# Kernel tuning notes

Measured on AMD Instinct MI355X. Metric: run time of the kernel, lower is better.

## Reference

```python
import jax, jax.numpy as jnp
import numpy as np

SIZE = 1024        # number of neurons
INPUT = 1024       # input_size (previous layer width)
CTX = 512          # context_size
CMS = 4            # context_map_size -> 2**4 = 16 weight rows per neuron
BATCH = 256
LR = 0.01
PCLIP = 0.01       # pred_clipping
WCLIP = 5.0        # weight_clipping


def _logit(x):
    return jnp.log(x) - jnp.log1p(-x)


def setup_inputs() -> dict:
    key = jax.random.key(0)
    k1, k2, k3, k4, k5, k6 = jax.random.split(key, 6)
    logits = jax.random.normal(k1, (INPUT, BATCH), jnp.float32)
    context_inputs = jax.random.normal(k2, (CTX, BATCH), jnp.float32)
    targets = jax.random.uniform(k3, (BATCH,), jnp.float32)
    context_maps = jax.random.normal(k4, (SIZE, CMS, CTX), jnp.float32)
    context_maps = context_maps / jnp.linalg.norm(context_maps, axis=2, keepdims=True)
    context_bias = jax.random.normal(k5, (SIZE, CMS, 1), jnp.float32)
    lo = _logit(jnp.float32(PCLIP))
    hi = _logit(jnp.float32(1.0 - PCLIP))
    bias = jax.random.uniform(k6, (1,), jnp.float32, lo, hi)
    weights = jnp.full((SIZE, 2 ** CMS, INPUT), 1.0 / INPUT, jnp.float32)
    return dict(logits=logits, context_inputs=context_inputs, targets=targets,
                weights=weights, context_maps=context_maps,
                context_bias=context_bias, bias=bias)


def reference(logits, context_inputs, targets, weights, context_maps, context_bias, bias):
    # --- context hashing: which of the 2^CMS weight rows each (neuron, sample) uses ---
    # distances: (size, cms, batch)
    distances = jnp.einsum('smc,cb->smb', context_maps, context_inputs)
    bits = (distances > context_bias).astype(jnp.int32)
    conv = (2 ** jnp.arange(CMS, dtype=jnp.int32))[None, :, None]
    idx = jnp.sum(bits * conv, axis=1)                 # (size, batch) in [0, 2^CMS)

    rows = jnp.arange(SIZE)[:, None]                   # (size, 1)
    sel = weights[rows, idx]                           # gathered weights (size, batch, input)

    lo = _logit(jnp.float32(PCLIP))
    hi = _logit(jnp.float32(1.0 - PCLIP))
    # torch does matmul(sel, logits).diagonal(dim1=1,dim2=2); the diagonal is exactly
    # the per-sample dot product, computed here directly without the (size,b,b) waste.
    out = jnp.clip(jnp.einsum('sbi,ib->sb', sel, logits), lo, hi)
    out = out.at[0].set(bias[0])                       # bias overrides neuron 0

    # --- online weight update (targets provided) ---
    sig = jax.nn.sigmoid(out)                          # (size, batch)
    upd = LR * (sig - targets[None, :])[:, :, None] * logits.T[None, :, :]  # (size,b,input)
    new_weights = weights.at[rows, idx].set(jnp.clip(sel - upd, -WCLIP, WCLIP))

    return jnp.squeeze(out), new_weights
```

## Files before the change

### kernel.cpp

```cpp
#include <hip/hip_runtime.h>

#define LRC   0.01f
#define WCLIP 5.0f
#define LO   (-4.5951198501345898f)
#define HI   ( 4.5951198501345898f)

__device__ __forceinline__ unsigned short f2bf(float f) {
    unsigned int u = __float_as_uint(f);
    u += 0x7fffu + ((u >> 16) & 1u);
    return (unsigned short)(u >> 16);
}
__device__ __forceinline__ float bflo(unsigned int p) { return __uint_as_float(p << 16); }
__device__ __forceinline__ float bfhi(unsigned int p) { return __uint_as_float(p & 0xffff0000u); }

__global__ __launch_bounds__(256) void k1_idx_lt(
    const float* __restrict__ cmap,
    const float* __restrict__ ctx,
    const float* __restrict__ cbias,
    const float* __restrict__ logits,
    int*   __restrict__ idxb,
    float* __restrict__ lT)
{
    __shared__ __align__(16) float As[64 * 68];
    __shared__ __align__(16) float Bs[64 * 68];
    const int t   = threadIdx.x;
    const int blk = blockIdx.x;

    if (blk < 256) {
        const int gm = blk >> 2, gn = blk & 3;
        const int m0 = gm << 6, n0 = gn << 6;
        const int tm = t >> 4, tn = t & 15;

        const int rs = t >> 4;
        const int cs = (t & 15) << 2;

        float acc[4][4];
        #pragma unroll
        for (int i = 0; i < 4; i++)
            #pragma unroll
            for (int j = 0; j < 4; j++) acc[i][j] = 0.f;

        float4 va[4], vb[4];
        #pragma unroll
        for (int rep = 0; rep < 4; rep++) {
            va[rep] = *(const float4*)(cmap + (m0 + (rep << 4) + rs) * 512 + cs);
            vb[rep] = *(const float4*)(ctx + (((rep << 4) + rs)) * 256 + n0 + cs);
        }

        for (int k0 = 0; k0 < 512; k0 += 64) {
            __syncthreads();
            #pragma unroll
            for (int rep = 0; rep < 4; rep++) {
                const int r = (rep << 4) + rs;
                As[(cs + 0) * 68 + r] = va[rep].x;
                As[(cs + 1) * 68 + r] = va[rep].y;
                As[(cs + 2) * 68 + r] = va[rep].z;
                As[(cs + 3) * 68 + r] = va[rep].w;
                *(float4*)(Bs + r * 68 + cs) = vb[rep];
            }
            if (k0 + 64 < 512) {
                #pragma unroll
                for (int rep = 0; rep < 4; rep++) {
                    va[rep] = *(const float4*)(cmap + (m0 + (rep << 4) + rs) * 512 + k0 + 64 + cs);
                    vb[rep] = *(const float4*)(ctx + (k0 + 64 + (rep << 4) + rs) * 256 + n0 + cs);
                }
            }
            __syncthreads();

            const float* ap = As + (tm << 2);
            const float* bp = Bs + (tn << 2);
            #pragma unroll 8
            for (int k = 0; k < 64; ++k) {
                float4 a4 = *(const float4*)(ap + k * 68);
                float4 b4 = *(const float4*)(bp + k * 68);
                acc[0][0] = fmaf(a4.x, b4.x, acc[0][0]);
                acc[0][1] = fmaf(a4.x, b4.y, acc[0][1]);
                acc[0][2] = fmaf(a4.x, b4.z, acc[0][2]);
                acc[0][3] = fmaf(a4.x, b4.w, acc[0][3]);
                acc[1][0] = fmaf(a4.y, b4.x, acc[1][0]);
                acc[1][1] = fmaf(a4.y, b4.y, acc[1][1]);
                acc[1][2] = fmaf(a4.y, b4.z, acc[1][2]);
                acc[1][3] = fmaf(a4.y, b4.w, acc[1][3]);
                acc[2][0] = fmaf(a4.z, b4.x, acc[2][0]);
                acc[2][1] = fmaf(a4.z, b4.y, acc[2][1]);
                acc[2][2] = fmaf(a4.z, b4.z, acc[2][2]);
                acc[2][3] = fmaf(a4.z, b4.w, acc[2][3]);
                acc[3][0] = fmaf(a4.w, b4.x, acc[3][0]);
                acc[3][1] = fmaf(a4.w, b4.y, acc[3][1]);
                acc[3][2] = fmaf(a4.w, b4.z, acc[3][2]);
                acc[3][3] = fmaf(a4.w, b4.w, acc[3][3]);
            }
        }
        const int s = (gm << 4) + tm;
        int4 iv;
        int* ivp = &iv.x;
        float cb[4];
        #pragma unroll
        for (int i = 0; i < 4; i++) cb[i] = cbias[(s << 2) + i];
        #pragma unroll
        for (int j = 0; j < 4; j++) {
            int v = 0;
            #pragma unroll
            for (int i = 0; i < 4; i++)
                v |= (acc[i][j] > cb[i]) ? (1 << i) : 0;
            ivp[j] = v;
        }
        *(int4*)(idxb + s * 256 + n0 + (tn << 2)) = iv;
    } else {
        float* T = As;
        const int bi = blk - 256;
        const int i0 = (bi >> 2) << 6;
        const int b0 = (bi & 3) << 6;
        #pragma unroll
        for (int rep = 0; rep < 4; rep++) {
            int flat4 = rep * 256 + t;
            int r = flat4 >> 4;
            int c = (flat4 & 15) << 2;
            float4 v = *(const float4*)(logits + (i0 + r) * 256 + b0 + c);
            T[(c + 0) * 68 + r] = v.x;
            T[(c + 1) * 68 + r] = v.y;
            T[(c + 2) * 68 + r] = v.z;
            T[(c + 3) * 68 + r] = v.w;
        }
        __syncthreads();
        #pragma unroll
        for (int rep = 0; rep < 4; rep++) {
            int flat4 = rep * 256 + t;
            int r = flat4 >> 4;
            int c = (flat4 & 15) << 2;
            *(float4*)(lT + (b0 + r) * 1024 + i0 + c) =
                *(const float4*)(T + r * 68 + c);
        }
    }
}

__global__ __launch_bounds__(1024) void k2_fwd_upd(
    const float* __restrict__ logits,
    const float* __restrict__ targets,
    const float* __restrict__ weights,
    const float* __restrict__ bias,
    const int*   __restrict__ idxb,
    const float* __restrict__ lT,
    float* __restrict__ outp,
    float* __restrict__ outw)
{
    __shared__ unsigned short wlds[64 * 68];
    __shared__ float red[3 * 4 * 256];
    __shared__ float sig_lds[4 * 256];
    __shared__ int   lastb[64];
    __shared__ float cf_lds[64];

    const int t  = threadIdx.x;
    const int b  = t & 255;
    const int q  = t >> 8;
    const int s0 = blockIdx.x << 2;

    if (t < 64) lastb[t] = -1;

    int jg[4], rowoff[4];
    #pragma unroll
    for (int g = 0; g < 4; g++) {
        jg[g] = idxb[(s0 + g) * 256 + b];
        rowoff[g] = ((g << 4) + jg[g]) * 68;
    }

    const int r   = t >> 4;
    const int c   = (t & 15) << 2;
    const float* wsrc = weights + ((s0 + (r >> 4)) << 14) + ((r & 15) << 10) + c;
    const int ldsoff = r * 68 + c;

    float4 pf = *(const float4*)wsrc;

    float acc[4] = {0.f, 0.f, 0.f, 0.f};
    const int qq = q << 4;

    for (int c0 = 0; c0 < 16; ++c0) {
        __syncthreads();
        unsigned int p0 = (unsigned int)f2bf(pf.x) | ((unsigned int)f2bf(pf.y) << 16);
        unsigned int p1 = (unsigned int)f2bf(pf.z) | ((unsigned int)f2bf(pf.w) << 16);
        *(uint2*)(wlds + ldsoff) = make_uint2(p0, p1);
        float4 nf;
        if (c0 < 15) nf = *(const float4*)(wsrc + ((c0 + 1) << 6));
        __syncthreads();

        const int ibase = (c0 << 6) + qq;
        #pragma unroll
        for (int ii = 0; ii < 16; ii += 4) {
            const int i = ibase + ii;
            float l0 = logits[(i + 0) * 256 + b];
            float l1 = logits[(i + 1) * 256 + b];
            float l2 = logits[(i + 2) * 256 + b];
            float l3 = logits[(i + 3) * 256 + b];
            #pragma unroll
            for (int g = 0; g < 4; g++) {
                uint2 wp = *(const uint2*)(wlds + rowoff[g] + qq + ii);
                acc[g] = fmaf(bflo(wp.x), l0, acc[g]);
                acc[g] = fmaf(bfhi(wp.x), l1, acc[g]);
                acc[g] = fmaf(bflo(wp.y), l2, acc[g]);
                acc[g] = fmaf(bfhi(wp.y), l3, acc[g]);
            }
        }
        pf = nf;
    }

    if (q > 0) {
        #pragma unroll
        for (int g = 0; g < 4; g++) red[((q - 1) * 4 + g) * 256 + b] = acc[g];
    }
    __syncthreads();
    if (q == 0) {
        #pragma unroll
        for (int g = 0; g < 4; g++) {
            float tot = acc[g] + red[(0 * 4 + g) * 256 + b]
                               + red[(1 * 4 + g) * 256 + b]
                               + red[(2 * 4 + g) * 256 + b];
            float outv = fminf(fmaxf(tot, LO), HI);
            if (s0 + g == 0) outv = bias[0];
            outp[(s0 + g) * 256 + b] = outv;
            sig_lds[(g << 8) + b] = 1.f / (1.f + __expf(-outv));
        }
    }
    __syncthreads();
    if (q == 0) {
        #pragma unroll
        for (int g = 0; g < 4; g++)
            atomicMax(&lastb[(g << 4) + jg[g]], b);
    }
    __syncthreads();
    if (t < 64) {
        int g  = t >> 4;
        int bb = lastb[t];
        float cfv = 0.f;
        if (bb >= 0) cfv = LRC * (sig_lds[(g << 8) + bb] - targets[bb]);
        cf_lds[t] = cfv;
    }
    __syncthreads();

    const int er = t >> 4;
    const int ec = (t & 15) << 2;
    const long rowbase = ((long)(s0 + (er >> 4)) << 14) + ((long)(er & 15) << 10);
    const int   col = lastb[er];
    const float cf  = cf_lds[er];
    const float* lrow = lT + ((long)(col < 0 ? 0 : col) << 10);
    #pragma unroll 4
    for (int seg = 0; seg < 16; ++seg) {
        const int c2 = ec + (seg << 6);
        float4 wv = *(const float4*)(weights + rowbase + c2);
        float4 res = wv;
        if (col >= 0) {
            float4 lv = *(const float4*)(lrow + c2);
            res.x = fminf(fmaxf(wv.x - cf * lv.x, -WCLIP), WCLIP);
            res.y = fminf(fmaxf(wv.y - cf * lv.y, -WCLIP), WCLIP);
            res.z = fminf(fmaxf(wv.z - cf * lv.z, -WCLIP), WCLIP);
            res.w = fminf(fmaxf(wv.w - cf * lv.w, -WCLIP), WCLIP);
        }
        *(float4*)(outw + rowbase + c2) = res;
    }
}

extern "C" void kernel_launch(void* const* d_in, const int* in_sizes, int n_in,
                              void* d_out, int out_size, void* d_ws, size_t ws_size,
                              hipStream_t stream) {
    const float* logits  = (const float*)d_in[0];
    const float* ctx     = (const float*)d_in[1];
    const float* targets = (const float*)d_in[2];
    const float* weights = (const float*)d_in[3];
    const float* cmap    = (const float*)d_in[4];
    const float* cbias   = (const float*)d_in[5];
    const float* bias    = (const float*)d_in[6];

    float* outp = (float*)d_out;
    float* outw = outp + 1024 * 256;

    char* ws = (char*)d_ws;
    int*   idxb = (int*)ws;
    float* lT   = (float*)(ws + (1 << 20));

    k1_idx_lt <<<320, 256, 0, stream>>>(cmap, ctx, cbias, logits, idxb, lT);
    k2_fwd_upd<<<256, 1024, 0, stream>>>(logits, targets, weights, bias, idxb,
                                         lT, outp, outw);
}
```

Measured before the change: 186.9 us.

## Split context GEMM along K into extra kernel and halve neurons per block

The context-distance GEMM is split along K into two halves across twice as many blocks. Partial sums are written to scratch space inside the output weight buffer, and a new second kernel sums them, computes the hash indices and transposes the logits. The forward/update kernel now handles 2 neurons per block instead of 4, doubling the grid to 512 blocks, with only half the threads staging weights. The aim is more parallelism on a GPU with many compute units, paid for by an extra launch and an extra round trip of partial sums through global memory.

```diff
diff --git a/kernel.cpp b/kernel.cpp
--- a/kernel.cpp
+++ b/kernel.cpp
@@ -13,101 +13,129 @@
 __device__ __forceinline__ float bflo(unsigned int p) { return __uint_as_float(p << 16); }
 __device__ __forceinline__ float bfhi(unsigned int p) { return __uint_as_float(p & 0xffff0000u); }
 
-__global__ __launch_bounds__(256) void k1_idx_lt(
+__global__ __launch_bounds__(256) void k1_part(
     const float* __restrict__ cmap,
     const float* __restrict__ ctx,
+    float* __restrict__ pd)
+{
+    __shared__ __align__(16) float As[64 * 68];
+    __shared__ __align__(16) float Bs[64 * 68];
+    const int t    = threadIdx.x;
+    const int tile = blockIdx.x >> 1;
+    const int kh   = blockIdx.x & 1;
+    const int kbase = kh << 8;
+
+    const int gm = tile >> 2, gn = tile & 3;
+    const int m0 = gm << 6, n0 = gn << 6;
+    const int tm = t >> 4, tn = t & 15;
+    const int rs = t >> 4;
+    const int cs = (t & 15) << 2;
+
+    float acc[4][4];
+    #pragma unroll
+    for (int i = 0; i < 4; i++)
+        #pragma unroll
+        for (int j = 0; j < 4; j++) acc[i][j] = 0.f;
+
+    float4 va[4], vb[4];
+    #pragma unroll
+    for (int rep = 0; rep < 4; rep++) {
+        va[rep] = *(const float4*)(cmap + (m0 + (rep << 4) + rs) * 512 + kbase + cs);
+        vb[rep] = *(const float4*)(ctx + (kbase + (rep << 4) + rs) * 256 + n0 + cs);
+    }
+
+    for (int k0 = kbase; k0 < kbase + 256; k0 += 64) {
+        __syncthreads();
+        #pragma unroll
+        for (int rep = 0; rep < 4; rep++) {
+            const int r = (rep << 4) + rs;
+            As[(cs + 0) * 68 + r] = va[rep].x;
+            As[(cs + 1) * 68 + r] = va[rep].y;
+            As[(cs + 2) * 68 + r] = va[rep].z;
+            As[(cs + 3) * 68 + r] = va[rep].w;
+            *(float4*)(Bs + r * 68 + cs) = vb[rep];
+        }
+        if (k0 + 64 < kbase + 256) {
+            #pragma unroll
+            for (int rep = 0; rep < 4; rep++) {
+                va[rep] = *(const float4*)(cmap + (m0 + (rep << 4) + rs) * 512 + k0 + 64 + cs);
+                vb[rep] = *(const float4*)(ctx + (k0 + 64 + (rep << 4) + rs) * 256 + n0 + cs);
+            }
+        }
+        __syncthreads();
+
+        const float* ap = As + (tm << 2);
+        const float* bp = Bs + (tn << 2);
+        #pragma unroll 8
+        for (int k = 0; k < 64; ++k) {
+            float4 a4 = *(const float4*)(ap + k * 68);
+            float4 b4 = *(const float4*)(bp + k * 68);
+            acc[0][0] = fmaf(a4.x, b4.x, acc[0][0]);
+            acc[0][1] = fmaf(a4.x, b4.y, acc[0][1]);
+            acc[0][2] = fmaf(a4.x, b4.z, acc[0][2]);
+            acc[0][3] = fmaf(a4.x, b4.w, acc[0][3]);
+            acc[1][0] = fmaf(a4.y, b4.x, acc[1][0]);
+            acc[1][1] = fmaf(a4.y, b4.y, acc[1][1]);
+            acc[1][2] = fmaf(a4.y, b4.z, acc[1][2]);
+            acc[1][3] = fmaf(a4.y, b4.w, acc[1][3]);
+            acc[2][0] = fmaf(a4.z, b4.x, acc[2][0]);
+            acc[2][1] = fmaf(a4.z, b4.y, acc[2][1]);
+            acc[2][2] = fmaf(a4.z, b4.z, acc[2][2]);
+            acc[2][3] = fmaf(a4.z, b4.w, acc[2][3]);
+            acc[3][0] = fmaf(a4.w, b4.x, acc[3][0]);
+            acc[3][1] = fmaf(a4.w, b4.y, acc[3][1]);
+            acc[3][2] = fmaf(a4.w, b4.z, acc[3][2]);
+            acc[3][3] = fmaf(a4.w, b4.w, acc[3][3]);
+        }
+    }
+    float* dst = pd + (kh ? (4096 * 256) : 0);
+    #pragma unroll
+    for (int i = 0; i < 4; i++) {
+        float4 v = make_float4(acc[i][0], acc[i][1], acc[i][2], acc[i][3]);
+        *(float4*)(dst + (m0 + (tm << 2) + i) * 256 + n0 + (tn << 2)) = v;
+    }
+}
+
+__global__ __launch_bounds__(256) void k1b_idx_lt(
+    const float* __restrict__ pd,
     const float* __restrict__ cbias,
     const float* __restrict__ logits,
     int*   __restrict__ idxb,
     float* __restrict__ lT)
 {
-    __shared__ __align__(16) float As[64 * 68];
-    __shared__ __align__(16) float Bs[64 * 68];
+    __shared__ float T[64 * 68];
     const int t   = threadIdx.x;
     const int blk = blockIdx.x;
 
     if (blk < 256) {
-        const int gm = blk >> 2, gn = blk & 3;
-        const int m0 = gm << 6, n0 = gn << 6;
-        const int tm = t >> 4, tn = t & 15;
-
-        const int rs = t >> 4;
-        const int cs = (t & 15) << 2;
-
-        float acc[4][4];
-        #pragma unroll
-        for (int i = 0; i < 4; i++)
-            #pragma unroll
-            for (int j = 0; j < 4; j++) acc[i][j] = 0.f;
-
-        float4 va[4], vb[4];
-        #pragma unroll
-        for (int rep = 0; rep < 4; rep++) {
-            va[rep] = *(const float4*)(cmap + (m0 + (rep << 4) + rs) * 512 + cs);
-            vb[rep] = *(const float4*)(ctx + (((rep << 4) + rs)) * 256 + n0 + cs);
-        }
-
-        for (int k0 = 0; k0 < 512; k0 += 64) {
-            __syncthreads();
-            #pragma unroll
-            for (int rep = 0; rep < 4; rep++) {
-                const int r = (rep << 4) + rs;
-                As[(cs + 0) * 68 + r] = va[rep].x;
-                As[(cs + 1) * 68 + r] = va[rep].y;
-                As[(cs + 2) * 68 + r] = va[rep].z;
-                As[(cs + 3) * 68 + r] = va[rep].w;
-                *(float4*)(Bs + r * 68 + cs) = vb[rep];
-            }
-            if (k0 + 64 < 512) {
-                #pragma unroll
-                for (int rep = 0; rep < 4; rep++) {
-                    va[rep] = *(const float4*)(cmap + (m0 + (rep << 4) + rs) * 512 + k0 + 64 + cs);
-                    vb[rep] = *(const float4*)(ctx + (k0 + 64 + (rep << 4) + rs) * 256 + n0 + cs);
-                }
-            }
-            __syncthreads();
-
-            const float* ap = As + (tm << 2);
-            const float* bp = Bs + (tn << 2);
-            #pragma unroll 8
-            for (int k = 0; k < 64; ++k) {
-                float4 a4 = *(const float4*)(ap + k * 68);
-                float4 b4 = *(const float4*)(bp + k * 68);
-                acc[0][0] = fmaf(a4.x, b4.x, acc[0][0]);
-                acc[0][1] = fmaf(a4.x, b4.y, acc[0][1]);
-                acc[0][2] = fmaf(a4.x, b4.z, acc[0][2]);
-                acc[0][3] = fmaf(a4.x, b4.w, acc[0][3]);
-                acc[1][0] = fmaf(a4.y, b4.x, acc[1][0]);
-                acc[1][1] = fmaf(a4.y, b4.y, acc[1][1]);
-                acc[1][2] = fmaf(a4.y, b4.z, acc[1][2]);
-                acc[1][3] = fmaf(a4.y, b4.w, acc[1][3]);
-                acc[2][0] = fmaf(a4.z, b4.x, acc[2][0]);
-                acc[2][1] = fmaf(a4.z, b4.y, acc[2][1]);
-                acc[2][2] = fmaf(a4.z, b4.z, acc[2][2]);
-                acc[2][3] = fmaf(a4.z, b4.w, acc[2][3]);
-                acc[3][0] = fmaf(a4.w, b4.x, acc[3][0]);
-                acc[3][1] = fmaf(a4.w, b4.y, acc[3][1]);
-                acc[3][2] = fmaf(a4.w, b4.z, acc[3][2]);
-                acc[3][3] = fmaf(a4.w, b4.w, acc[3][3]);
-            }
-        }
-        const int s = (gm << 4) + tm;
+        const int sg = (blk << 2) + (t >> 6);
+        const int c4 = (t & 63) << 2;
         int4 iv;
         int* ivp = &iv.x;
+        float d[4][4];
+        #pragma unroll
+        for (int i = 0; i < 4; i++) {
+            const int m = (sg << 2) + i;
+            float4 p0 = *(const float4*)(pd + m * 256 + c4);
+            float4 p1 = *(const float4*)(pd + 4096 * 256 + m * 256 + c4);
+            d[i][0] = p0.x + p1.x;
+            d[i][1] = p0.y + p1.y;
+            d[i][2] = p0.z + p1.z;
+            d[i][3] = p0.w + p1.w;
+        }
         float cb[4];
         #pragma unroll
-        for (int i = 0; i < 4; i++) cb[i] = cbias[(s << 2) + i];
+        for (int i = 0; i < 4; i++) cb[i] = cbias[(sg << 2) + i];
         #pragma unroll
         for (int j = 0; j < 4; j++) {
             int v = 0;
             #pragma unroll
             for (int i = 0; i < 4; i++)
-                v |= (acc[i][j] > cb[i]) ? (1 << i) : 0;
+                v |= (d[i][j] > cb[i]) ? (1 << i) : 0;
             ivp[j] = v;
         }
-        *(int4*)(idxb + s * 256 + n0 + (tn << 2)) = iv;
+        *(int4*)(idxb + sg * 256 + c4) = iv;
     } else {
-        float* T = As;
         const int bi = blk - 256;
         const int i0 = (bi >> 2) << 6;
         const int b0 = (bi & 3) << 6;
@@ -144,43 +172,46 @@
     float* __restrict__ outp,
     float* __restrict__ outw)
 {
-    __shared__ unsigned short wlds[64 * 68];
-    __shared__ float red[3 * 4 * 256];
-    __shared__ float sig_lds[4 * 256];
-    __shared__ int   lastb[64];
-    __shared__ float cf_lds[64];
+    __shared__ unsigned short wlds[32 * 68];
+    __shared__ float red[3 * 2 * 256];
+    __shared__ float sig_lds[2 * 256];
+    __shared__ int   lastb[32];
+    __shared__ float cf_lds[32];
 
     const int t  = threadIdx.x;
     const int b  = t & 255;
     const int q  = t >> 8;
-    const int s0 = blockIdx.x << 2;
-
-    if (t < 64) lastb[t] = -1;
-
-    int jg[4], rowoff[4];
+    const int s0 = blockIdx.x << 1;
+
+    if (t < 32) lastb[t] = -1;
+
+    int jg[2], rowoff[2];
     #pragma unroll
-    for (int g = 0; g < 4; g++) {
+    for (int g = 0; g < 2; g++) {
         jg[g] = idxb[(s0 + g) * 256 + b];
         rowoff[g] = ((g << 4) + jg[g]) * 68;
     }
 
-    const int r   = t >> 4;
-    const int c   = (t & 15) << 2;
+    const int r = t >> 4;
+    const int c = (t & 15) << 2;
     const float* wsrc = weights + ((s0 + (r >> 4)) << 14) + ((r & 15) << 10) + c;
     const int ldsoff = r * 68 + c;
-
-    float4 pf = *(const float4*)wsrc;
-
-    float acc[4] = {0.f, 0.f, 0.f, 0.f};
+    const bool stager = (t < 512);
+
+    float4 pf;
+    if (stager) pf = *(const float4*)wsrc;
+
+    float acc[2] = {0.f, 0.f};
     const int qq = q << 4;
 
     for (int c0 = 0; c0 < 16; ++c0) {
         __syncthreads();
-        unsigned int p0 = (unsigned int)f2bf(pf.x) | ((unsigned int)f2bf(pf.y) << 16);
-        unsigned int p1 = (unsigned int)f2bf(pf.z) | ((unsigned int)f2bf(pf.w) << 16);
-        *(uint2*)(wlds + ldsoff) = make_uint2(p0, p1);
-        float4 nf;
-        if (c0 < 15) nf = *(const float4*)(wsrc + ((c0 + 1) << 6));
+        if (stager) {
+            unsigned int p0 = (unsigned int)f2bf(pf.x) | ((unsigned int)f2bf(pf.y) << 16);
+            unsigned int p1 = (unsigned int)f2bf(pf.z) | ((unsigned int)f2bf(pf.w) << 16);
+            *(uint2*)(wlds + ldsoff) = make_uint2(p0, p1);
+            if (c0 < 15) pf = *(const float4*)(wsrc + ((c0 + 1) << 6));
+        }
         __syncthreads();
 
         const int ibase = (c0 << 6) + qq;
@@ -192,7 +223,7 @@
             float l2 = logits[(i + 2) * 256 + b];
             float l3 = logits[(i + 3) * 256 + b];
             #pragma unroll
-            for (int g = 0; g < 4; g++) {
+            for (int g = 0; g < 2; g++) {
                 uint2 wp = *(const uint2*)(wlds + rowoff[g] + qq + ii);
                 acc[g] = fmaf(bflo(wp.x), l0, acc[g]);
                 acc[g] = fmaf(bfhi(wp.x), l1, acc[g]);
@@ -200,20 +231,19 @@
                 acc[g] = fmaf(bfhi(wp.y), l3, acc[g]);
             }
         }
-        pf = nf;
     }
 
     if (q > 0) {
         #pragma unroll
-        for (int g = 0; g < 4; g++) red[((q - 1) * 4 + g) * 256 + b] = acc[g];
+        for (int g = 0; g < 2; g++) red[((q - 1) * 2 + g) * 256 + b] = acc[g];
     }
     __syncthreads();
     if (q == 0) {
         #pragma unroll
-        for (int g = 0; g < 4; g++) {
-            float tot = acc[g] + red[(0 * 4 + g) * 256 + b]
-                               + red[(1 * 4 + g) * 256 + b]
-                               + red[(2 * 4 + g) * 256 + b];
+        for (int g = 0; g < 2; g++) {
+            float tot = acc[g] + red[(0 * 2 + g) * 256 + b]
+                               + red[(1 * 2 + g) * 256 + b]
+                               + red[(2 * 2 + g) * 256 + b];
             float outv = fminf(fmaxf(tot, LO), HI);
             if (s0 + g == 0) outv = bias[0];
             outp[(s0 + g) * 256 + b] = outv;
@@ -223,11 +253,11 @@
     __syncthreads();
     if (q == 0) {
         #pragma unroll
-        for (int g = 0; g < 4; g++)
+        for (int g = 0; g < 2; g++)
             atomicMax(&lastb[(g << 4) + jg[g]], b);
     }
     __syncthreads();
-    if (t < 64) {
+    if (t < 32) {
         int g  = t >> 4;
         int bb = lastb[t];
         float cfv = 0.f;
@@ -236,15 +266,15 @@
     }
     __syncthreads();
 
-    const int er = t >> 4;
-    const int ec = (t & 15) << 2;
+    const int er = t >> 5;
+    const int ec = (t & 31) << 2;
     const long rowbase = ((long)(s0 + (er >> 4)) << 14) + ((long)(er & 15) << 10);
     const int   col = lastb[er];
     const float cf  = cf_lds[er];
     const float* lrow = lT + ((long)(col < 0 ? 0 : col) << 10);
     #pragma unroll 4
-    for (int seg = 0; seg < 16; ++seg) {
-        const int c2 = ec + (seg << 6);
+    for (int seg = 0; seg < 8; ++seg) {
+        const int c2 = ec + (seg << 7);
         float4 wv = *(const float4*)(weights + rowbase + c2);
         float4 res = wv;
         if (col >= 0) {
@@ -276,7 +306,10 @@
     int*   idxb = (int*)ws;
     float* lT   = (float*)(ws + (1 << 20));
 
-    k1_idx_lt <<<320, 256, 0, stream>>>(cmap, ctx, cbias, logits, idxb, lT);
-    k2_fwd_upd<<<256, 1024, 0, stream>>>(logits, targets, weights, bias, idxb,
+    float* pd = outw;
+
+    k1_part   <<<512, 256, 0, stream>>>(cmap, ctx, pd);
+    k1b_idx_lt<<<320, 256, 0, stream>>>(pd, cbias, logits, idxb, lT);
+    k2_fwd_upd<<<512, 1024, 0, stream>>>(logits, targets, weights, bias, idxb,
                                          lT, outp, outw);
 }
```

Result: slower. 217.6 us (+16.5%).

## Split-K context GEMM, two-phase staged forward, separate row-parallel weight update

Applied to the files above, without the earlier changes.

The context-distance GEMM is split four ways along K across 1024 blocks. Partial sums go to scratch held in the output-weights buffer, and the forward kernel reduces them and computes the hash bits itself. The forward kernel now stages weights into an XOR-swizzled LDS buffer in two halves, replacing 16 small chunks and cutting barriers, and reads 16-byte bf16 vectors. The weight update moves to its own kernel with 4096 blocks, so the large copy and update traffic gets more parallelism, at the cost of an extra launch and extra scratch traffic for the partial sums.

```diff
diff --git a/kernel.cpp b/kernel.cpp
--- a/kernel.cpp
+++ b/kernel.cpp
@@ -13,12 +13,11 @@
 __device__ __forceinline__ float bflo(unsigned int p) { return __uint_as_float(p << 16); }
 __device__ __forceinline__ float bfhi(unsigned int p) { return __uint_as_float(p & 0xffff0000u); }
 
-__global__ __launch_bounds__(256) void k1_idx_lt(
+__global__ __launch_bounds__(256) void k1_part(
     const float* __restrict__ cmap,
     const float* __restrict__ ctx,
-    const float* __restrict__ cbias,
     const float* __restrict__ logits,
-    int*   __restrict__ idxb,
+    float* __restrict__ pd,
     float* __restrict__ lT)
 {
     __shared__ __align__(16) float As[64 * 68];
@@ -26,11 +25,14 @@
     const int t   = threadIdx.x;
     const int blk = blockIdx.x;
 
-    if (blk < 256) {
-        const int gm = blk >> 2, gn = blk & 3;
+    if (blk < 1024) {
+        const int tile  = blk >> 2;
+        const int kq    = blk & 3;
+        const int kbase = kq << 7;
+
+        const int gm = tile >> 2, gn = tile & 3;
         const int m0 = gm << 6, n0 = gn << 6;
         const int tm = t >> 4, tn = t & 15;
-
         const int rs = t >> 4;
         const int cs = (t & 15) << 2;
 
@@ -43,11 +45,11 @@
         float4 va[4], vb[4];
         #pragma unroll
         for (int rep = 0; rep < 4; rep++) {
-            va[rep] = *(const float4*)(cmap + (m0 + (rep << 4) + rs) * 512 + cs);
-            vb[rep] = *(const float4*)(ctx + (((rep << 4) + rs)) * 256 + n0 + cs);
-        }
-
-        for (int k0 = 0; k0 < 512; k0 += 64) {
+            va[rep] = *(const float4*)(cmap + (m0 + (rep << 4) + rs) * 512 + kbase + cs);
+            vb[rep] = *(const float4*)(ctx + (kbase + (rep << 4) + rs) * 256 + n0 + cs);
+        }
+
+        for (int k0 = kbase; k0 < kbase + 128; k0 += 64) {
             __syncthreads();
             #pragma unroll
             for (int rep = 0; rep < 4; rep++) {
@@ -58,7 +60,7 @@
                 As[(cs + 3) * 68 + r] = va[rep].w;
                 *(float4*)(Bs + r * 68 + cs) = vb[rep];
             }
-            if (k0 + 64 < 512) {
+            if (k0 + 64 < kbase + 128) {
                 #pragma unroll
                 for (int rep = 0; rep < 4; rep++) {
                     va[rep] = *(const float4*)(cmap + (m0 + (rep << 4) + rs) * 512 + k0 + 64 + cs);
@@ -91,24 +93,15 @@
                 acc[3][3] = fmaf(a4.w, b4.w, acc[3][3]);
             }
         }
-        const int s = (gm << 4) + tm;
-        int4 iv;
-        int* ivp = &iv.x;
-        float cb[4];
-        #pragma unroll
-        for (int i = 0; i < 4; i++) cb[i] = cbias[(s << 2) + i];
-        #pragma unroll
-        for (int j = 0; j < 4; j++) {
-            int v = 0;
-            #pragma unroll
-            for (int i = 0; i < 4; i++)
-                v |= (acc[i][j] > cb[i]) ? (1 << i) : 0;
-            ivp[j] = v;
-        }
-        *(int4*)(idxb + s * 256 + n0 + (tn << 2)) = iv;
+        float* dst = pd + (long)kq * (4096 * 256);
+        #pragma unroll
+        for (int i = 0; i < 4; i++) {
+            float4 v = make_float4(acc[i][0], acc[i][1], acc[i][2], acc[i][3]);
+            *(float4*)(dst + (m0 + (tm << 2) + i) * 256 + n0 + (tn << 2)) = v;
+        }
     } else {
         float* T = As;
-        const int bi = blk - 256;
+        const int bi = blk - 1024;
         const int i0 = (bi >> 2) << 6;
         const int b0 = (bi & 3) << 6;
         #pragma unroll
@@ -134,75 +127,119 @@
     }
 }
 
-__global__ __launch_bounds__(1024) void k2_fwd_upd(
+__global__ __launch_bounds__(1024, 4) void k2a_fwd(
     const float* __restrict__ logits,
     const float* __restrict__ targets,
     const float* __restrict__ weights,
     const float* __restrict__ bias,
-    const int*   __restrict__ idxb,
-    const float* __restrict__ lT,
+    const float* __restrict__ cbias,
+    const float* __restrict__ pd,
     float* __restrict__ outp,
-    float* __restrict__ outw)
+    float* __restrict__ coefb,
+    int*   __restrict__ colb)
 {
-    __shared__ unsigned short wlds[64 * 68];
-    __shared__ float red[3 * 4 * 256];
-    __shared__ float sig_lds[4 * 256];
-    __shared__ int   lastb[64];
-    __shared__ float cf_lds[64];
+    __shared__ __align__(16) unsigned short wlds[64 * 512];
+    float* red  = (float*)wlds;
+    float* sig  = (float*)wlds + 3072;
+    int*   lastb = (int*)((float*)wlds + 4096);
 
     const int t  = threadIdx.x;
     const int b  = t & 255;
     const int q  = t >> 8;
     const int s0 = blockIdx.x << 2;
 
+    const int r  = t >> 4;
+    const int c  = (t & 15) << 2;
+    const float* wsrc = weights + ((s0 + (r >> 4)) << 14) + ((r & 15) << 10) + c;
+    const int swz     = (r & 15) << 3;
+    const int ldsbase = r << 9;
+
+    float4 pf[8];
+    #pragma unroll
+    for (int seg = 0; seg < 8; ++seg)
+        pf[seg] = *(const float4*)(wsrc + (seg << 6));
+
+    int jg[4], rowoff[4], gswz[4];
+    #pragma unroll
+    for (int g = 0; g < 4; g++) {
+        int v = 0;
+        #pragma unroll
+        for (int mm = 0; mm < 4; mm++) {
+            const float* pp = pd + ((s0 + g) * 4 + mm) * 256 + b;
+            float d = ((pp[0] + pp[4096 * 256]) + pp[2 * 4096 * 256]) + pp[3 * 4096 * 256];
+            v |= (d > cbias[(s0 + g) * 4 + mm]) ? (1 << mm) : 0;
+        }
+        jg[g] = v;
+        rowoff[g] = ((g << 4) + v) << 9;
+        gswz[g]   = v << 3;
+    }
+
+    #pragma unroll
+    for (int seg = 0; seg < 8; ++seg) {
+        unsigned int p0 = (unsigned int)f2bf(pf[seg].x) | ((unsigned int)f2bf(pf[seg].y) << 16);
+        unsigned int p1 = (unsigned int)f2bf(pf[seg].z) | ((unsigned int)f2bf(pf[seg].w) << 16);
+        *(uint2*)(wlds + ldsbase + (((seg << 6) + c) ^ swz)) = make_uint2(p0, p1);
+    }
+    __syncthreads();
+
+    #pragma unroll
+    for (int seg = 0; seg < 8; ++seg)
+        pf[seg] = *(const float4*)(wsrc + 512 + (seg << 6));
+
+    float acc[4] = {0.f, 0.f, 0.f, 0.f};
+    const int qq = q << 7;
+
+    #pragma unroll 4
+    for (int ii = 0; ii < 128; ii += 8) {
+        const int il = qq + ii;
+        float l[8];
+        #pragma unroll
+        for (int u = 0; u < 8; ++u) l[u] = logits[(il + u) * 256 + b];
+        #pragma unroll
+        for (int g = 0; g < 4; g++) {
+            uint4 wp = *(const uint4*)(wlds + rowoff[g] + (il ^ gswz[g]));
+            acc[g] = fmaf(bflo(wp.x), l[0], acc[g]);
+            acc[g] = fmaf(bfhi(wp.x), l[1], acc[g]);
+            acc[g] = fmaf(bflo(wp.y), l[2], acc[g]);
+            acc[g] = fmaf(bfhi(wp.y), l[3], acc[g]);
+            acc[g] = fmaf(bflo(wp.z), l[4], acc[g]);
+            acc[g] = fmaf(bfhi(wp.z), l[5], acc[g]);
+            acc[g] = fmaf(bflo(wp.w), l[6], acc[g]);
+            acc[g] = fmaf(bfhi(wp.w), l[7], acc[g]);
+        }
+    }
+    __syncthreads();
+
+    #pragma unroll
+    for (int seg = 0; seg < 8; ++seg) {
+        unsigned int p0 = (unsigned int)f2bf(pf[seg].x) | ((unsigned int)f2bf(pf[seg].y) << 16);
+        unsigned int p1 = (unsigned int)f2bf(pf[seg].z) | ((unsigned int)f2bf(pf[seg].w) << 16);
+        *(uint2*)(wlds + ldsbase + (((seg << 6) + c) ^ swz)) = make_uint2(p0, p1);
+    }
+    __syncthreads();
+
+    #pragma unroll 4
+    for (int ii = 0; ii < 128; ii += 8) {
+        const int il = qq + ii;
+        float l[8];
+        #pragma unroll
+        for (int u = 0; u < 8; ++u) l[u] = logits[(512 + il + u) * 256 + b];
+        #pragma unroll
+        for (int g = 0; g < 4; g++) {
+            uint4 wp = *(const uint4*)(wlds + rowoff[g] + (il ^ gswz[g]));
+            acc[g] = fmaf(bflo(wp.x), l[0], acc[g]);
+            acc[g] = fmaf(bfhi(wp.x), l[1], acc[g]);
+            acc[g] = fmaf(bflo(wp.y), l[2], acc[g]);
+            acc[g] = fmaf(bfhi(wp.y), l[3], acc[g]);
+            acc[g] = fmaf(bflo(wp.z), l[4], acc[g]);
+            acc[g] = fmaf(bfhi(wp.z), l[5], acc[g]);
+            acc[g] = fmaf(bflo(wp.w), l[6], acc[g]);
+            acc[g] = fmaf(bfhi(wp.w), l[7], acc[g]);
+        }
+    }
+    __syncthreads();
+
     if (t < 64) lastb[t] = -1;
-
-    int jg[4], rowoff[4];
-    #pragma unroll
-    for (int g = 0; g < 4; g++) {
-        jg[g] = idxb[(s0 + g) * 256 + b];
-        rowoff[g] = ((g << 4) + jg[g]) * 68;
-    }
-
-    const int r   = t >> 4;
-    const int c   = (t & 15) << 2;
-    const float* wsrc = weights + ((s0 + (r >> 4)) << 14) + ((r & 15) << 10) + c;
-    const int ldsoff = r * 68 + c;
-
-    float4 pf = *(const float4*)wsrc;
-
-    float acc[4] = {0.f, 0.f, 0.f, 0.f};
-    const int qq = q << 4;
-
-    for (int c0 = 0; c0 < 16; ++c0) {
-        __syncthreads();
-        unsigned int p0 = (unsigned int)f2bf(pf.x) | ((unsigned int)f2bf(pf.y) << 16);
-        unsigned int p1 = (unsigned int)f2bf(pf.z) | ((unsigned int)f2bf(pf.w) << 16);
-        *(uint2*)(wlds + ldsoff) = make_uint2(p0, p1);
-        float4 nf;
-        if (c0 < 15) nf = *(const float4*)(wsrc + ((c0 + 1) << 6));
-        __syncthreads();
-
-        const int ibase = (c0 << 6) + qq;
-        #pragma unroll
-        for (int ii = 0; ii < 16; ii += 4) {
-            const int i = ibase + ii;
-            float l0 = logits[(i + 0) * 256 + b];
-            float l1 = logits[(i + 1) * 256 + b];
-            float l2 = logits[(i + 2) * 256 + b];
-            float l3 = logits[(i + 3) * 256 + b];
-            #pragma unroll
-            for (int g = 0; g < 4; g++) {
-                uint2 wp = *(const uint2*)(wlds + rowoff[g] + qq + ii);
-                acc[g] = fmaf(bflo(wp.x), l0, acc[g]);
-                acc[g] = fmaf(bfhi(wp.x), l1, acc[g]);
-                acc[g] = fmaf(bflo(wp.y), l2, acc[g]);
-                acc[g] = fmaf(bfhi(wp.y), l3, acc[g]);
-            }
-        }
-        pf = nf;
-    }
-
     if (q > 0) {
         #pragma unroll
         for (int g = 0; g < 4; g++) red[((q - 1) * 4 + g) * 256 + b] = acc[g];
@@ -217,7 +254,7 @@
             float outv = fminf(fmaxf(tot, LO), HI);
             if (s0 + g == 0) outv = bias[0];
             outp[(s0 + g) * 256 + b] = outv;
-            sig_lds[(g << 8) + b] = 1.f / (1.f + __expf(-outv));
+            sig[(g << 8) + b] = 1.f / (1.f + __expf(-outv));
         }
     }
     __syncthreads();
@@ -231,30 +268,37 @@
         int g  = t >> 4;
         int bb = lastb[t];
         float cfv = 0.f;
-        if (bb >= 0) cfv = LRC * (sig_lds[(g << 8) + bb] - targets[bb]);
-        cf_lds[t] = cfv;
-    }
-    __syncthreads();
-
-    const int er = t >> 4;
-    const int ec = (t & 15) << 2;
-    const long rowbase = ((long)(s0 + (er >> 4)) << 14) + ((long)(er & 15) << 10);
-    const int   col = lastb[er];
-    const float cf  = cf_lds[er];
-    const float* lrow = lT + ((long)(col < 0 ? 0 : col) << 10);
-    #pragma unroll 4
-    for (int seg = 0; seg < 16; ++seg) {
-        const int c2 = ec + (seg << 6);
-        float4 wv = *(const float4*)(weights + rowbase + c2);
+        if (bb >= 0) cfv = LRC * (sig[(g << 8) + bb] - targets[bb]);
+        coefb[(s0 << 4) + t] = cfv;
+        colb [(s0 << 4) + t] = bb;
+    }
+}
+
+__global__ __launch_bounds__(256) void k2b_update(
+    const float* __restrict__ weights,
+    const float* __restrict__ lT,
+    const float* __restrict__ coefb,
+    const int*   __restrict__ colb,
+    float* __restrict__ outw)
+{
+    const int t  = threadIdx.x;
+    const int r0 = blockIdx.x << 2;
+    const int o  = t << 2;
+    #pragma unroll
+    for (int rr = 0; rr < 4; rr++) {
+        const int row = r0 + rr;
+        const int col = colb[row];
+        const float cf = coefb[row];
+        float4 wv = *(const float4*)(weights + (long)row * 1024 + o);
         float4 res = wv;
         if (col >= 0) {
-            float4 lv = *(const float4*)(lrow + c2);
+            float4 lv = *(const float4*)(lT + (long)col * 1024 + o);
             res.x = fminf(fmaxf(wv.x - cf * lv.x, -WCLIP), WCLIP);
             res.y = fminf(fmaxf(wv.y - cf * lv.y, -WCLIP), WCLIP);
             res.z = fminf(fmaxf(wv.z - cf * lv.z, -WCLIP), WCLIP);
             res.w = fminf(fmaxf(wv.w - cf * lv.w, -WCLIP), WCLIP);
         }
-        *(float4*)(outw + rowbase + c2) = res;
+        *(float4*)(outw + (long)row * 1024 + o) = res;
     }
 }
 
@@ -273,10 +317,14 @@
     float* outw = outp + 1024 * 256;
 
     char* ws = (char*)d_ws;
-    int*   idxb = (int*)ws;
-    float* lT   = (float*)(ws + (1 << 20));
-
-    k1_idx_lt <<<320, 256, 0, stream>>>(cmap, ctx, cbias, logits, idxb, lT);
-    k2_fwd_upd<<<256, 1024, 0, stream>>>(logits, targets, weights, bias, idxb,
-                                         lT, outp, outw);
-}
+    float* lT    = (float*)ws;
+    float* coefb = (float*)(ws + (1 << 20));
+    int*   colb  = (int*)  (ws + (1 << 20) + (1 << 16));
+
+    float* pd = outw;
+
+    k1_part   <<<1088, 256, 0, stream>>>(cmap, ctx, logits, pd, lT);
+    k2a_fwd   <<<256, 1024, 0, stream>>>(logits, targets, weights, bias,
+                                         cbias, pd, outp, coefb, colb);
+    k2b_update<<<4096, 256, 0, stream>>>(weights, lT, coefb, colb, outw);
+}
```

Result: slower. 198.9 us (+6.5%).
